# Optimization experiments

Hardware: AMD Instinct MI355X
Metric: run time of the kernel (lower is better)

Reference implementation:

```python
import jax, jax.numpy as jnp
import numpy as np

IN_CHANNELS = 3
WINDOW_SIZE = 11
SIGMA = 1.5
PAD = WINDOW_SIZE // 2


def _create_window():
    # NOTE: faithful to the original repo, the exponent is POSITIVE (a known
    # bug in AntixK/PyTorch-VAE); we replicate the exact math.
    x = np.arange(WINDOW_SIZE, dtype=np.float64)
    k = np.exp((x - WINDOW_SIZE // 2) ** 2 / (2.0 * SIGMA ** 2))
    k = (k / k.sum()).astype(np.float32)
    w2d = np.outer(k, k)  # [K, K]
    # depthwise kernel, OIHW with groups=C -> [C, 1, K, K]
    return jnp.asarray(np.broadcast_to(w2d, (IN_CHANNELS, 1, WINDOW_SIZE, WINDOW_SIZE)).copy())


def _dwconv(x, w):
    return jax.lax.conv_general_dilated(
        x, w, window_strides=(1, 1), padding=[(PAD, PAD), (PAD, PAD)],
        feature_group_count=IN_CHANNELS,
        dimension_numbers=('NCHW', 'OIHW', 'NCHW'))


def _avg_pool2(x):
    B, C, H, W = x.shape
    return x.reshape(B, C, H // 2, 2, W // 2, 2).mean(axis=(3, 5))


def _ssim(img1, img2, window):
    mu1 = _dwconv(img1, window)
    mu2 = _dwconv(img2, window)
    mu1_sq = mu1 * mu1
    mu2_sq = mu2 * mu2
    mu1_mu2 = mu1 * mu2
    sigma1_sq = _dwconv(img1 * img1, window) - mu1_sq
    sigma2_sq = _dwconv(img2 * img2, window) - mu2_sq
    sigma12 = _dwconv(img1 * img2, window) - mu1_mu2
    C1 = 0.01 ** 2
    C2 = 0.03 ** 2
    v1 = 2.0 * sigma12 + C2
    v2 = sigma1_sq + sigma2_sq + C2
    cs = jnp.mean(v1 / v2)
    ssim_map = (2.0 * mu1_mu2 + C1) * v1 / ((mu1_sq + mu2_sq + C1) * v2)
    return jnp.mean(ssim_map), cs  # size_average=True


def setup_inputs() -> dict:
    key = jax.random.key(0)
    k1, k2 = jax.random.split(key)
    shape = (32, 3, 512, 512)
    img1 = jax.random.uniform(k1, shape, dtype=jnp.float32)
    img2 = jax.random.uniform(k2, shape, dtype=jnp.float32)
    return {"img1": img1, "img2": img2}


def reference(img1, img2):
    weights = jnp.asarray([0.0448, 0.2856, 0.3001, 0.2363, 0.1333], dtype=jnp.float32)
    window = _create_window()
    mssim, mcs = [], []
    for _ in range(5):
        sim, cs = _ssim(img1, img2, window)
        mssim.append(sim)
        mcs.append(cs)
        img1 = _avg_pool2(img1)
        img2 = _avg_pool2(img2)
    mssim = jnp.stack(mssim)
    mcs = jnp.stack(mcs)
    pow1 = mcs ** weights
    pow2 = mssim ** weights
    output = jnp.prod(pow1[:-1] * pow2[-1])
    return 1.0 - output
```

## Files before the change

kernel.cpp:

```cpp
#include <hip/hip_runtime.h>
#include <cmath>

typedef short bf16x8 __attribute__((ext_vector_type(8)));
typedef float f32x4 __attribute__((ext_vector_type(4)));

struct Coeffs { float k[11]; };

__device__ __forceinline__ ushort f2bf(float f) {
    unsigned u = __float_as_uint(f);
    u += 0x7fff + ((u >> 16) & 1);
    return (ushort)(u >> 16);
}

__device__ __forceinline__ unsigned pk2(float lo, float hi) {
    unsigned d;
    asm("v_cvt_pk_bf16_f32 %0, %1, %2" : "=v"(d) : "v"(lo), "v"(hi));
    return d;
}

__device__ __forceinline__ float frcp(float x) { return __builtin_amdgcn_rcpf(x); }

__device__ __forceinline__ float4 ld4s(const float* __restrict__ p, int r, int c, int H, int W) {
    float4 v = make_float4(0.f, 0.f, 0.f, 0.f);
    if (r >= 0 && r < H) {
        const float* row = p + (size_t)r * W;
        if (c >= 0 && c + 3 < W) {
            v = *reinterpret_cast<const float4*>(row + c);
        } else {
            if (c + 0 >= 0 && c + 0 < W) v.x = row[c + 0];
            if (c + 1 >= 0 && c + 1 < W) v.y = row[c + 1];
            if (c + 2 >= 0 && c + 2 < W) v.z = row[c + 2];
            if (c + 3 >= 0 && c + 3 < W) v.w = row[c + 3];
        }
    }
    return v;
}

union FragU { ushort us[8]; bf16x8 v; uint4 q; };
union RdU   { uint4 q; bf16x8 v; };

__global__ __launch_bounds__(64)
void init_frag_kernel(uint4* __restrict__ tab, Coeffs cf) {
    const int lane = threadIdx.x;
    const int lj   = lane & 15;
    const int part = lane >> 4;
    FragU bHf, aVf;
    #pragma unroll
    for (int i = 0; i < 8; ++i) {
        const int kk = part * 8 + i;
        const int tH = kk - lj - 3;
        const int tV = kk - lj;
        float vH = 0.f, vV = 0.f;
        #pragma unroll
        for (int tt = 0; tt < 11; ++tt) {
            vH = (tH == tt) ? cf.k[tt] : vH;
            vV = (tV == tt) ? cf.k[tt] : vV;
        }
        bHf.us[i] = f2bf(vH);
        aVf.us[i] = f2bf(vV);
    }
    tab[lane]      = bHf.q;
    tab[64 + lane] = aVf.q;
}

__global__ __launch_bounds__(256)
void ssim_level0_mfma(const float* __restrict__ i1, const float* __restrict__ i2,
                      float* __restrict__ o1, float* __restrict__ o2,
                      int H, int W,
                      double* __restrict__ accum,
                      const uint4* __restrict__ frag_tab)
{
    __shared__ __align__(16) ushort A_lds[2][48][64];
    __shared__ __align__(16) ushort H_T [5][32][64];
    __shared__ double red[2][4];

    const int tid  = threadIdx.x;
    const int lane = tid & 63;
    const int lj   = lane & 15;
    const int part = lane >> 4;
    const int swz  = (lane & 7) << 4;
    const int wv   = __builtin_amdgcn_readfirstlane(tid) >> 6;

    const int bc = blockIdx.z;
    const int r0 = blockIdx.y * 32;
    const int c0 = blockIdx.x * 32;
    const float* p1 = i1 + (size_t)bc * H * W;
    const float* p2 = i2 + (size_t)bc * H * W;

    RdU bHu, aVu;
    bHu.q = frag_tab[lane];
    aVu.q = frag_tab[64 + lane];
    const bf16x8 bH = bHu.v;
    const bf16x8 aV = aVu.v;

    if (tid < 192) {
        const int row_rel = tid >> 2;
        const int colg    = tid & 3;
        const int gr  = r0 - 5 + row_rel;
        const int gc0 = c0 - 8 + 12 * colg;

        float a[12], b[12];
        if (gr >= 0 && gr < H && gc0 >= 0 && gc0 + 12 <= W) {
            const size_t idx = (size_t)gr * W + gc0;
            const float* pa = p1 + idx;
            const float* pb = p2 + idx;
            #pragma unroll
            for (int g = 0; g < 3; ++g) {
                float4 va = *reinterpret_cast<const float4*>(pa + 4 * g);
                float4 vb = *reinterpret_cast<const float4*>(pb + 4 * g);
                a[4*g+0]=va.x; a[4*g+1]=va.y; a[4*g+2]=va.z; a[4*g+3]=va.w;
                b[4*g+0]=vb.x; b[4*g+1]=vb.y; b[4*g+2]=vb.z; b[4*g+3]=vb.w;
            }
        } else {
            #pragma unroll
            for (int g = 0; g < 3; ++g) {
                float4 va = ld4s(p1, gr, gc0 + 4 * g, H, W);
                float4 vb = ld4s(p2, gr, gc0 + 4 * g, H, W);
                a[4*g+0]=va.x; a[4*g+1]=va.y; a[4*g+2]=va.z; a[4*g+3]=va.w;
                b[4*g+0]=vb.x; b[4*g+1]=vb.y; b[4*g+2]=vb.z; b[4*g+3]=vb.w;
            }
        }

        unsigned pks[2][6];
        #pragma unroll
        for (int e = 0; e < 6; ++e) {
            pks[0][e] = pk2(a[2*e], a[2*e+1]);
            pks[1][e] = pk2(b[2*e], b[2*e+1]);
        }
        const int cb   = 24 * colg;
        const int swzr = (row_rel & 7) << 4;
        char* base0 = (char*)&A_lds[0][0][0] + row_rel * 128;
        char* q0 = base0 + ((cb)      ^ swzr);
        char* q1 = base0 + ((cb + 8)  ^ swzr);
        char* q2 = base0 + ((cb + 16) ^ swzr);
        #pragma unroll
        for (int s = 0; s < 2; ++s) {
            *(uint2*)(q0 + s * 6144) = make_uint2(pks[s][0], pks[s][1]);
            *(uint2*)(q1 + s * 6144) = make_uint2(pks[s][2], pks[s][3]);
            *(uint2*)(q2 + s * 6144) = make_uint2(pks[s][4], pks[s][5]);
        }
    } else if (o1 != nullptr) {
        const int p = tid - 192;
        const int i = p & 15;
        const int h = p >> 4;
        const size_t idx = (size_t)(r0 + 2 * i) * W + (c0 + 8 * h);
        const float* pa = p1 + idx;
        const float* pb = p2 + idx;
        float4 a00 = *reinterpret_cast<const float4*>(pa);
        float4 a01 = *reinterpret_cast<const float4*>(pa + 4);
        float4 a10 = *reinterpret_cast<const float4*>(pa + W);
        float4 a11 = *reinterpret_cast<const float4*>(pa + W + 4);
        float4 b00 = *reinterpret_cast<const float4*>(pb);
        float4 b01 = *reinterpret_cast<const float4*>(pb + 4);
        float4 b10 = *reinterpret_cast<const float4*>(pb + W);
        float4 b11 = *reinterpret_cast<const float4*>(pb + W + 4);
        float4 oa, ob;
        oa.x = 0.25f*(a00.x+a00.y+a10.x+a10.y); oa.y = 0.25f*(a00.z+a00.w+a10.z+a10.w);
        oa.z = 0.25f*(a01.x+a01.y+a11.x+a11.y); oa.w = 0.25f*(a01.z+a01.w+a11.z+a11.w);
        ob.x = 0.25f*(b00.x+b00.y+b10.x+b10.y); ob.y = 0.25f*(b00.z+b00.w+b10.z+b10.w);
        ob.z = 0.25f*(b01.x+b01.y+b11.x+b11.y); ob.w = 0.25f*(b01.z+b01.w+b11.z+b11.w);
        const int W2 = W >> 1;
        const size_t base = (size_t)bc * (size_t)(H >> 1) * W2
                          + (size_t)(r0/2 + i) * W2 + (c0/2 + 4*h);
        *reinterpret_cast<float4*>(o1 + base) = oa;
        *reinterpret_cast<float4*>(o2 + base) = ob;
    }
    __syncthreads();

    const f32x4 zf = {0.f, 0.f, 0.f, 0.f};
    if (wv < 3) {
        const char* Ab = (const char*)&A_lds[0][0][0] + wv * 2048 + lj * 128;
        const char* a0p = Ab + ((part * 16)      ^ swz);
        const char* a1p = Ab + ((32 + part * 16) ^ swz);
        char* st = (char*)&H_T[0][0][0] + lj * 128 + ((wv * 32 + part * 8) ^ swz);
        #pragma unroll
        for (int cg = 0; cg < 2; ++cg) {
            const char* ap = cg ? a1p : a0p;
            uint4 da = *(const uint4*)(ap);
            uint4 db = *(const uint4*)(ap + 6144);
            unsigned wa[4] = {da.x, da.y, da.z, da.w};
            unsigned wb[4] = {db.x, db.y, db.z, db.w};
            uint4 qaa, qbb, qab;
            unsigned* paa = &qaa.x; unsigned* pbb = &qbb.x; unsigned* pab = &qab.x;
            #pragma unroll
            for (int e = 0; e < 4; ++e) {
                const float alo = __uint_as_float(wa[e] << 16);
                const float ahi = __uint_as_float(wa[e] & 0xffff0000u);
                const float blo = __uint_as_float(wb[e] << 16);
                const float bhi = __uint_as_float(wb[e] & 0xffff0000u);
                paa[e] = pk2(alo * alo, ahi * ahi);
                pbb[e] = pk2(blo * blo, bhi * bhi);
                pab[e] = pk2(alo * blo, ahi * bhi);
            }
            RdU f0, f1, f2, f3, f4;
            f0.q = da; f1.q = db; f2.q = qaa; f3.q = qbb; f4.q = qab;
            f32x4 d0 = __builtin_amdgcn_mfma_f32_16x16x32_bf16(f0.v, bH, zf, 0, 0, 0);
            f32x4 d1 = __builtin_amdgcn_mfma_f32_16x16x32_bf16(f1.v, bH, zf, 0, 0, 0);
            f32x4 d2 = __builtin_amdgcn_mfma_f32_16x16x32_bf16(f2.v, bH, zf, 0, 0, 0);
            f32x4 d3 = __builtin_amdgcn_mfma_f32_16x16x32_bf16(f3.v, bH, zf, 0, 0, 0);
            f32x4 d4 = __builtin_amdgcn_mfma_f32_16x16x32_bf16(f4.v, bH, zf, 0, 0, 0);
            char* sc = st + cg * 2048;
            *(uint2*)(sc)          = make_uint2(pk2(d0[0], d0[1]), pk2(d0[2], d0[3]));
            *(uint2*)(sc + 4096)   = make_uint2(pk2(d1[0], d1[1]), pk2(d1[2], d1[3]));
            *(uint2*)(sc + 8192)   = make_uint2(pk2(d2[0], d2[1]), pk2(d2[2], d2[3]));
            *(uint2*)(sc + 12288)  = make_uint2(pk2(d3[0], d3[1]), pk2(d3[2], d3[3]));
            *(uint2*)(sc + 16384)  = make_uint2(pk2(d4[0], d4[1]), pk2(d4[2], d4[3]));
        }
    }
    __syncthreads();

    const int rg2 = wv >> 1;
    const int cg2 = wv & 1;
    const char* hb = (const char*)&H_T[0][0][0] + cg2 * 2048 + lj * 128
                   + ((rg2 * 32 + part * 16) ^ swz);
    f32x4 acc[5];
    #pragma unroll
    for (int s = 0; s < 5; ++s) {
        RdU br;
        br.q = *(const uint4*)(hb + s * 4096);
        acc[s] = __builtin_amdgcn_mfma_f32_16x16x32_bf16(aV, br.v, zf, 0, 0, 0);
    }

    const float C1 = 1e-4f, C2 = 9e-4f;
    float ssim_acc = 0.f, cs_acc = 0.f;
    #pragma unroll
    for (int r = 0; r < 4; ++r) {
        const float mu1 = acc[0][r], mu2 = acc[1][r];
        const float m11 = acc[2][r], m22 = acc[3][r], m12 = acc[4][r];
        const float mu1s = mu1 * mu1, mu2s = mu2 * mu2, mu12 = mu1 * mu2;
        const float v1 = 2.f * (m12 - mu12) + C2;
        const float v2 = (m11 - mu1s) + (m22 - mu2s) + C2;
        const float r2 = frcp(v2);
        const float rd = frcp(mu1s + mu2s + C1);
        cs_acc   += v1 * r2;
        ssim_acc += (2.f * mu12 + C1) * v1 * r2 * rd;
    }

    #pragma unroll
    for (int off = 32; off > 0; off >>= 1) {
        ssim_acc += __shfl_down(ssim_acc, off);
        cs_acc   += __shfl_down(cs_acc, off);
    }
    if (lane == 0) { red[0][wv] = (double)ssim_acc; red[1][wv] = (double)cs_acc; }
    __syncthreads();
    if (tid == 0) {
        double s = red[0][0] + red[0][1] + red[0][2] + red[0][3];
        double c = red[1][0] + red[1][1] + red[1][2] + red[1][3];
        int slot = (blockIdx.x + blockIdx.y * 3 + blockIdx.z * 7) & 63;
        atomicAdd(&accum[slot], s);
        atomicAdd(&accum[64 + slot], c);
    }
}

__global__ __launch_bounds__(256)
void ssim_level1_mfma(const float* __restrict__ i1, const float* __restrict__ i2,
                      float* __restrict__ o1, float* __restrict__ o2,
                      int H, int W,
                      double* __restrict__ accum,
                      const uint4* __restrict__ frag_tab)
{
    __shared__ __align__(16) ushort H_T[5][32][64];
    __shared__ double red[2][4];

    const int tid  = threadIdx.x;
    const int lane = tid & 63;
    const int lj   = lane & 15;
    const int part = lane >> 4;
    const int swz  = (lane & 7) << 4;
    const int wv   = __builtin_amdgcn_readfirstlane(tid) >> 6;

    const int bc = blockIdx.z;
    const int r0 = blockIdx.y * 32;
    const int c0 = blockIdx.x * 32;
    const float* p1 = i1 + (size_t)bc * H * W;
    const float* p2 = i2 + (size_t)bc * H * W;

    RdU bHu, aVu;
    bHu.q = frag_tab[lane];
    aVu.q = frag_tab[64 + lane];
    const bf16x8 bH = bHu.v;
    const bf16x8 aV = aVu.v;

    const f32x4 zf = {0.f, 0.f, 0.f, 0.f};

    if (wv < 3) {
        const int gr = r0 - 5 + wv * 16 + lj;
        char* st = (char*)&H_T[0][0][0] + lj * 128 + ((wv * 32 + part * 8) ^ swz);
        #pragma unroll
        for (int cg = 0; cg < 2; ++cg) {
            const int gc = c0 - 8 + cg * 16 + part * 8;
            float a8[8], b8[8];
            if (gr >= 0 && gr < H && gc >= 0 && gc + 8 <= W) {
                const size_t idx = (size_t)gr * W + gc;
                float4 va0 = *reinterpret_cast<const float4*>(p1 + idx);
                float4 va1 = *reinterpret_cast<const float4*>(p1 + idx + 4);
                float4 vb0 = *reinterpret_cast<const float4*>(p2 + idx);
                float4 vb1 = *reinterpret_cast<const float4*>(p2 + idx + 4);
                a8[0]=va0.x; a8[1]=va0.y; a8[2]=va0.z; a8[3]=va0.w;
                a8[4]=va1.x; a8[5]=va1.y; a8[6]=va1.z; a8[7]=va1.w;
                b8[0]=vb0.x; b8[1]=vb0.y; b8[2]=vb0.z; b8[3]=vb0.w;
                b8[4]=vb1.x; b8[5]=vb1.y; b8[6]=vb1.z; b8[7]=vb1.w;
            } else {
                float4 va0 = ld4s(p1, gr, gc, H, W);
                float4 va1 = ld4s(p1, gr, gc + 4, H, W);
                float4 vb0 = ld4s(p2, gr, gc, H, W);
                float4 vb1 = ld4s(p2, gr, gc + 4, H, W);
                a8[0]=va0.x; a8[1]=va0.y; a8[2]=va0.z; a8[3]=va0.w;
                a8[4]=va1.x; a8[5]=va1.y; a8[6]=va1.z; a8[7]=va1.w;
                b8[0]=vb0.x; b8[1]=vb0.y; b8[2]=vb0.z; b8[3]=vb0.w;
                b8[4]=vb1.x; b8[5]=vb1.y; b8[6]=vb1.z; b8[7]=vb1.w;
            }

            unsigned pkf[5][4];
            #pragma unroll
            for (int e = 0; e < 4; ++e) {
                const float a0 = a8[2*e], a1 = a8[2*e+1];
                const float b0 = b8[2*e], b1 = b8[2*e+1];
                pkf[0][e] = pk2(a0, a1);
                pkf[1][e] = pk2(b0, b1);
                pkf[2][e] = pk2(a0*a0, a1*a1);
                pkf[3][e] = pk2(b0*b0, b1*b1);
                pkf[4][e] = pk2(a0*b0, a1*b1);
            }
            #pragma unroll
            for (int s = 0; s < 5; ++s) {
                RdU fr;
                fr.q.x = pkf[s][0]; fr.q.y = pkf[s][1];
                fr.q.z = pkf[s][2]; fr.q.w = pkf[s][3];
                f32x4 d = __builtin_amdgcn_mfma_f32_16x16x32_bf16(fr.v, bH, zf, 0, 0, 0);
                *(uint2*)(st + cg * 2048 + s * 4096)
                    = make_uint2(pk2(d[0], d[1]), pk2(d[2], d[3]));
            }
        }
    } else if (o1 != nullptr) {
        const int p = tid - 192;
        const int i = p & 15;
        const int h = p >> 4;
        const size_t idx = (size_t)(r0 + 2 * i) * W + (c0 + 8 * h);
        const float* pa = p1 + idx;
        const float* pb = p2 + idx;
        float4 a00 = *reinterpret_cast<const float4*>(pa);
        float4 a01 = *reinterpret_cast<const float4*>(pa + 4);
        float4 a10 = *reinterpret_cast<const float4*>(pa + W);
        float4 a11 = *reinterpret_cast<const float4*>(pa + W + 4);
        float4 b00 = *reinterpret_cast<const float4*>(pb);
        float4 b01 = *reinterpret_cast<const float4*>(pb + 4);
        float4 b10 = *reinterpret_cast<const float4*>(pb + W);
        float4 b11 = *reinterpret_cast<const float4*>(pb + W + 4);
        float4 oa, ob;
        oa.x = 0.25f*(a00.x+a00.y+a10.x+a10.y); oa.y = 0.25f*(a00.z+a00.w+a10.z+a10.w);
        oa.z = 0.25f*(a01.x+a01.y+a11.x+a11.y); oa.w = 0.25f*(a01.z+a01.w+a11.z+a11.w);
        ob.x = 0.25f*(b00.x+b00.y+b10.x+b10.y); ob.y = 0.25f*(b00.z+b00.w+b10.z+b10.w);
        ob.z = 0.25f*(b01.x+b01.y+b11.x+b11.y); ob.w = 0.25f*(b01.z+b01.w+b11.z+b11.w);
        const int W2 = W >> 1;
        const size_t base = (size_t)bc * (size_t)(H >> 1) * W2
                          + (size_t)(r0/2 + i) * W2 + (c0/2 + 4*h);
        *reinterpret_cast<float4*>(o1 + base) = oa;
        *reinterpret_cast<float4*>(o2 + base) = ob;
    }
    __syncthreads();

    const int rg2 = wv >> 1;
    const int cg2 = wv & 1;
    const char* hb = (const char*)&H_T[0][0][0] + cg2 * 2048 + lj * 128
                   + ((rg2 * 32 + part * 16) ^ swz);
    f32x4 acc[5];
    #pragma unroll
    for (int s = 0; s < 5; ++s) {
        RdU br;
        br.q = *(const uint4*)(hb + s * 4096);
        acc[s] = __builtin_amdgcn_mfma_f32_16x16x32_bf16(aV, br.v, zf, 0, 0, 0);
    }

    const float C1 = 1e-4f, C2 = 9e-4f;
    float ssim_acc = 0.f, cs_acc = 0.f;
    #pragma unroll
    for (int r = 0; r < 4; ++r) {
        const float mu1 = acc[0][r], mu2 = acc[1][r];
        const float m11 = acc[2][r], m22 = acc[3][r], m12 = acc[4][r];
        const float mu1s = mu1 * mu1, mu2s = mu2 * mu2, mu12 = mu1 * mu2;
        const float v1 = 2.f * (m12 - mu12) + C2;
        const float v2 = (m11 - mu1s) + (m22 - mu2s) + C2;
        const float r2 = frcp(v2);
        const float rd = frcp(mu1s + mu2s + C1);
        cs_acc   += v1 * r2;
        ssim_acc += (2.f * mu12 + C1) * v1 * r2 * rd;
    }

    #pragma unroll
    for (int off = 32; off > 0; off >>= 1) {
        ssim_acc += __shfl_down(ssim_acc, off);
        cs_acc   += __shfl_down(cs_acc, off);
    }
    if (lane == 0) { red[0][wv] = (double)ssim_acc; red[1][wv] = (double)cs_acc; }
    __syncthreads();
    if (tid == 0) {
        double s = red[0][0] + red[0][1] + red[0][2] + red[0][3];
        double c = red[1][0] + red[1][1] + red[1][2] + red[1][3];
        int slot = (blockIdx.x + blockIdx.y * 3 + blockIdx.z * 7) & 63;
        atomicAdd(&accum[slot], s);
        atomicAdd(&accum[64 + slot], c);
    }
}

#define SPF 33
#define HRF 42

__global__ __launch_bounds__(256)
void ssim_level_f32(const float* __restrict__ i1, const float* __restrict__ i2,
                    float* __restrict__ o1, float* __restrict__ o2,
                    int H, int W,
                    double* __restrict__ accum, Coeffs cf)
{
    __shared__ __align__(16) float varr[5][HRF][SPF];
    __shared__ __align__(16) float phl[2][16][16];
    __shared__ double red[2][4];

    const int tid = threadIdx.x;
    const int bc  = blockIdx.z;
    const int r0 = blockIdx.y * 32;
    const int c0 = blockIdx.x * 32;
    const float* p1 = i1 + (size_t)bc * H * W;
    const float* p2 = i2 + (size_t)bc * H * W;

    const int row_rel = tid >> 2;
    const int j  = tid & 3;
    const int cl = 8 * j;
    float hpA[4], hpB[4];
    bool pool_thread = false;

    if (tid < HRF * 4) {
        const int gr  = r0 + row_rel - 5;
        const int gcb = c0 + cl - 8;

        float a[24], b[24];
        if (gr >= 0 && gr < H && gcb >= 0 && gcb + 24 <= W) {
            const size_t idx = (size_t)gr * W + gcb;
            const float* pa = p1 + idx;
            const float* pb = p2 + idx;
            #pragma unroll
            for (int g = 0; g < 6; ++g) {
                float4 va = *reinterpret_cast<const float4*>(pa + 4 * g);
                float4 vb = *reinterpret_cast<const float4*>(pb + 4 * g);
                a[4*g+0]=va.x; a[4*g+1]=va.y; a[4*g+2]=va.z; a[4*g+3]=va.w;
                b[4*g+0]=vb.x; b[4*g+1]=vb.y; b[4*g+2]=vb.z; b[4*g+3]=vb.w;
            }
        } else {
            #pragma unroll
            for (int g = 0; g < 6; ++g) {
                float4 va = ld4s(p1, gr, gcb + 4 * g, H, W);
                float4 vb = ld4s(p2, gr, gcb + 4 * g, H, W);
                a[4*g+0]=va.x; a[4*g+1]=va.y; a[4*g+2]=va.z; a[4*g+3]=va.w;
                b[4*g+0]=vb.x; b[4*g+1]=vb.y; b[4*g+2]=vb.z; b[4*g+3]=vb.w;
            }
        }

        float acc[5][8] = {};
        #pragma unroll
        for (int i = 0; i < 24; ++i) {
            float av = a[i], bv = b[i];
            float pa2 = av * av, pb2 = bv * bv, pab = av * bv;
            #pragma unroll
            for (int jo = 0; jo < 8; ++jo) {
                const int t = i - 3 - jo;
                if (t >= 0 && t <= 10) {
                    const float kk = cf.k[t];
                    acc[0][jo] += kk * av;  acc[1][jo] += kk * bv;
                    acc[2][jo] += kk * pa2; acc[3][jo] += kk * pb2;
                    acc[4][jo] += kk * pab;
                }
            }
        }
        #pragma unroll
        for (int s = 0; s < 5; ++s) {
            *reinterpret_cast<float4*>(&varr[s][row_rel][cl]) =
                make_float4(acc[s][0], acc[s][1], acc[s][2], acc[s][3]);
            *reinterpret_cast<float4*>(&varr[s][row_rel][cl + 4]) =
                make_float4(acc[s][4], acc[s][5], acc[s][6], acc[s][7]);
        }

        if (o1 != nullptr && row_rel >= 5 && row_rel <= 36) {
            #pragma unroll
            for (int p = 0; p < 4; ++p) {
                hpA[p] = a[8 + 2*p] + a[9 + 2*p];
                hpB[p] = b[8 + 2*p] + b[9 + 2*p];
            }
            if (row_rel & 1) {
                const int i = (row_rel - 5) >> 1;
                *reinterpret_cast<float4*>(&phl[0][i][4*j]) = make_float4(hpA[0],hpA[1],hpA[2],hpA[3]);
                *reinterpret_cast<float4*>(&phl[1][i][4*j]) = make_float4(hpB[0],hpB[1],hpB[2],hpB[3]);
            } else if (row_rel >= 6) {
                pool_thread = true;
            }
        }
    }
    __syncthreads();

    if (pool_thread) {
        const int i = (row_rel - 6) >> 1;
        const int W2 = W >> 1;
        float4 qa = *reinterpret_cast<const float4*>(&phl[0][i][4*j]);
        float4 qb = *reinterpret_cast<const float4*>(&phl[1][i][4*j]);
        qa.x = 0.25f*(qa.x + hpA[0]); qa.y = 0.25f*(qa.y + hpA[1]);
        qa.z = 0.25f*(qa.z + hpA[2]); qa.w = 0.25f*(qa.w + hpA[3]);
        qb.x = 0.25f*(qb.x + hpB[0]); qb.y = 0.25f*(qb.y + hpB[1]);
        qb.z = 0.25f*(qb.z + hpB[2]); qb.w = 0.25f*(qb.w + hpB[3]);
        const size_t base = (size_t)bc * (size_t)(H >> 1) * W2
                          + (size_t)(r0/2 + i) * W2 + (c0/2 + 4*j);
        *reinterpret_cast<float4*>(o1 + base) = qa;
        *reinterpret_cast<float4*>(o2 + base) = qb;
    }

    const int col = tid & 31;
    const int rg  = tid >> 5;

    float acc[5][4] = {};
    #pragma unroll
    for (int t = 0; t < 14; ++t) {
        const int m = rg * 4 + t;
        #pragma unroll
        for (int s = 0; s < 5; ++s) {
            const float val = varr[s][m][col];
            #pragma unroll
            for (int i = 0; i < 4; ++i) {
                const int tap = t - i;
                if (tap >= 0 && tap <= 10) acc[s][i] += cf.k[tap] * val;
            }
        }
    }

    const float C1 = 1e-4f, C2 = 9e-4f;
    float ssim_acc = 0.f, cs_acc = 0.f;
    #pragma unroll
    for (int i = 0; i < 4; ++i) {
        const float mu1 = acc[0][i], mu2 = acc[1][i];
        const float m11 = acc[2][i], m22 = acc[3][i], m12 = acc[4][i];
        const float mu1s = mu1 * mu1, mu2s = mu2 * mu2, mu12 = mu1 * mu2;
        const float v1 = 2.f * (m12 - mu12) + C2;
        const float v2 = (m11 - mu1s) + (m22 - mu2s) + C2;
        const float r2 = frcp(v2);
        const float rd = frcp(mu1s + mu2s + C1);
        cs_acc   += v1 * r2;
        ssim_acc += (2.f * mu12 + C1) * v1 * r2 * rd;
    }

    #pragma unroll
    for (int off = 32; off > 0; off >>= 1) {
        ssim_acc += __shfl_down(ssim_acc, off);
        cs_acc   += __shfl_down(cs_acc, off);
    }
    const int wave = tid >> 6, lane = tid & 63;
    if (lane == 0) { red[0][wave] = (double)ssim_acc; red[1][wave] = (double)cs_acc; }
    __syncthreads();
    if (tid == 0) {
        double s = red[0][0] + red[0][1] + red[0][2] + red[0][3];
        double c = red[1][0] + red[1][1] + red[1][2] + red[1][3];
        int slot = (blockIdx.x + blockIdx.y * 3 + blockIdx.z * 7) & 63;
        atomicAdd(&accum[slot], s);
        atomicAdd(&accum[64 + slot], c);
    }
}

__global__ __launch_bounds__(64)
void finalize_kernel(const double* __restrict__ accum,
                     float* __restrict__ out, int BC)
{
    __shared__ double sums[5][2];
    int tid = threadIdx.x;
    for (int lvl = 0; lvl < 5; ++lvl) {
        for (int m = 0; m < 2; ++m) {
            double v = accum[(lvl * 2 + m) * 64 + tid];
            for (int off = 32; off > 0; off >>= 1) v += __shfl_down(v, off);
            if (tid == 0) sums[lvl][m] = v;
        }
    }
    __syncthreads();
    if (tid == 0) {
        const double w[5] = {0.0448, 0.2856, 0.3001, 0.2363, 0.1333};
        double prod = 1.0;
        for (int lvl = 0; lvl < 5; ++lvl) {
            int hw = (512 >> lvl);
            double cnt = (double)BC * (double)hw * (double)hw;
            double mssim = sums[lvl][0] / cnt;
            double mcs   = sums[lvl][1] / cnt;
            if (lvl < 4) {
                prod *= pow(mcs, w[lvl]);
            } else {
                double p2 = pow(mssim, w[4]);
                prod *= p2 * p2 * p2 * p2;
            }
        }
        out[0] = (float)(1.0 - prod);
    }
}

extern "C" void kernel_launch(void* const* d_in, const int* in_sizes, int n_in,
                              void* d_out, int out_size, void* d_ws, size_t ws_size,
                              hipStream_t stream) {
    const float* img1 = (const float*)d_in[0];
    const float* img2 = (const float*)d_in[1];
    float* out = (float*)d_out;
    char* ws = (char*)d_ws;

    const int BC = in_sizes[0] / (512 * 512);

    double* accum = (double*)ws;
    uint4*  ftab  = (uint4*)(ws + 6144);
    size_t off = 8192;
    float* lvl1[5] = {nullptr, nullptr, nullptr, nullptr, nullptr};
    float* lvl2[5] = {nullptr, nullptr, nullptr, nullptr, nullptr};
    for (int l = 1; l < 5; ++l) {
        size_t hw = (size_t)(512 >> l) * (512 >> l);
        lvl1[l] = (float*)(ws + off); off += (size_t)BC * hw * sizeof(float);
        lvl2[l] = (float*)(ws + off); off += (size_t)BC * hw * sizeof(float);
    }

    hipMemsetAsync(accum, 0, 5 * 2 * 64 * sizeof(double), stream);

    Coeffs cf;
    {
        double kd[11], sum = 0.0;
        for (int i = 0; i < 11; ++i) { kd[i] = exp(((double)((i-5)*(i-5))) / 4.5); sum += kd[i]; }
        for (int i = 0; i < 11; ++i) cf.k[i] = (float)(kd[i] / sum);
    }

    init_frag_kernel<<<1, 64, 0, stream>>>(ftab, cf);

    const float* cur1 = img1;
    const float* cur2 = img2;
    for (int lvl = 0; lvl < 5; ++lvl) {
        int H = 512 >> lvl, W = H;
        dim3 grid(W / 32, H / 32, BC);
        float* n1 = (lvl < 4) ? lvl1[lvl + 1] : nullptr;
        float* n2 = (lvl < 4) ? lvl2[lvl + 1] : nullptr;
        if (lvl == 0) {
            ssim_level0_mfma<<<grid, 256, 0, stream>>>(cur1, cur2, n1, n2, H, W,
                                                       accum + lvl * 128, ftab);
        } else if (lvl == 1) {
            ssim_level1_mfma<<<grid, 256, 0, stream>>>(cur1, cur2, n1, n2, H, W,
                                                       accum + lvl * 128, ftab);
        } else {
            ssim_level_f32<<<grid, 256, 0, stream>>>(cur1, cur2, n1, n2, H, W,
                                                     accum + lvl * 128, cf);
        }
        cur1 = n1; cur2 = n2;
    }

    finalize_kernel<<<1, 64, 0, stream>>>(accum, out, BC);
}
```

Baseline: 181.3 us.

## Process two 32-column tiles per level-0 block with software-pipelined staging

The level-0 SSIM kernel now handles a 32x64 region per block, two 32x32 tiles in sequence, and launches half as many blocks along x. The second tile's global loads are issued up front and held in registers. They are written to LDS while the vertical MFMA pass of the first tile runs, which overlaps load latency with compute. This amortizes per-block setup (fragment table loads, reduction, atomics) over more work, but raises register pressure, adds extra barriers, and halves the block count, which can reduce occupancy.

After: 160.4 us. -11.6%, faster.

```diff
diff --git a/kernel.cpp b/kernel.cpp
--- a/kernel.cpp
+++ b/kernel.cpp
@@ -63,6 +63,136 @@
     tab[64 + lane] = aVf.q;
 }
 
+__device__ __forceinline__ void stage_load(const float* __restrict__ p1,
+                                           const float* __restrict__ p2,
+                                           int H, int W, int gr, int gc0,
+                                           float (&a)[12], float (&b)[12]) {
+    if (gr >= 0 && gr < H && gc0 >= 0 && gc0 + 12 <= W) {
+        const size_t idx = (size_t)gr * W + gc0;
+        #pragma unroll
+        for (int g = 0; g < 3; ++g) {
+            float4 va = *reinterpret_cast<const float4*>(p1 + idx + 4 * g);
+            float4 vb = *reinterpret_cast<const float4*>(p2 + idx + 4 * g);
+            a[4*g+0]=va.x; a[4*g+1]=va.y; a[4*g+2]=va.z; a[4*g+3]=va.w;
+            b[4*g+0]=vb.x; b[4*g+1]=vb.y; b[4*g+2]=vb.z; b[4*g+3]=vb.w;
+        }
+    } else {
+        #pragma unroll
+        for (int g = 0; g < 3; ++g) {
+            float4 va = ld4s(p1, gr, gc0 + 4 * g, H, W);
+            float4 vb = ld4s(p2, gr, gc0 + 4 * g, H, W);
+            a[4*g+0]=va.x; a[4*g+1]=va.y; a[4*g+2]=va.z; a[4*g+3]=va.w;
+            b[4*g+0]=vb.x; b[4*g+1]=vb.y; b[4*g+2]=vb.z; b[4*g+3]=vb.w;
+        }
+    }
+}
+
+__device__ __forceinline__ void stage_write(const float (&a)[12], const float (&b)[12],
+                                            char* q0, char* q1, char* q2) {
+    unsigned pks[2][6];
+    #pragma unroll
+    for (int e = 0; e < 6; ++e) {
+        pks[0][e] = pk2(a[2*e], a[2*e+1]);
+        pks[1][e] = pk2(b[2*e], b[2*e+1]);
+    }
+    #pragma unroll
+    for (int s = 0; s < 2; ++s) {
+        *(uint2*)(q0 + s * 6144) = make_uint2(pks[s][0], pks[s][1]);
+        *(uint2*)(q1 + s * 6144) = make_uint2(pks[s][2], pks[s][3]);
+        *(uint2*)(q2 + s * 6144) = make_uint2(pks[s][4], pks[s][5]);
+    }
+}
+
+__device__ __forceinline__ void h_phase(const char* a0p, const char* a1p, char* st,
+                                        const bf16x8 bH, const f32x4 zf) {
+    #pragma unroll
+    for (int cg = 0; cg < 2; ++cg) {
+        const char* ap = cg ? a1p : a0p;
+        uint4 da = *(const uint4*)(ap);
+        uint4 db = *(const uint4*)(ap + 6144);
+        unsigned wa[4] = {da.x, da.y, da.z, da.w};
+        unsigned wb[4] = {db.x, db.y, db.z, db.w};
+        uint4 qaa, qbb, qab;
+        unsigned* paa = &qaa.x; unsigned* pbb = &qbb.x; unsigned* pab = &qab.x;
+        #pragma unroll
+        for (int e = 0; e < 4; ++e) {
+            const float alo = __uint_as_float(wa[e] << 16);
+            const float ahi = __uint_as_float(wa[e] & 0xffff0000u);
+            const float blo = __uint_as_float(wb[e] << 16);
+            const float bhi = __uint_as_float(wb[e] & 0xffff0000u);
+            paa[e] = pk2(alo * alo, ahi * ahi);
+            pbb[e] = pk2(blo * blo, bhi * bhi);
+            pab[e] = pk2(alo * blo, ahi * bhi);
+        }
+        RdU f0, f1, f2, f3, f4;
+        f0.q = da; f1.q = db; f2.q = qaa; f3.q = qbb; f4.q = qab;
+        f32x4 d0 = __builtin_amdgcn_mfma_f32_16x16x32_bf16(f0.v, bH, zf, 0, 0, 0);
+        f32x4 d1 = __builtin_amdgcn_mfma_f32_16x16x32_bf16(f1.v, bH, zf, 0, 0, 0);
+        f32x4 d2 = __builtin_amdgcn_mfma_f32_16x16x32_bf16(f2.v, bH, zf, 0, 0, 0);
+        f32x4 d3 = __builtin_amdgcn_mfma_f32_16x16x32_bf16(f3.v, bH, zf, 0, 0, 0);
+        f32x4 d4 = __builtin_amdgcn_mfma_f32_16x16x32_bf16(f4.v, bH, zf, 0, 0, 0);
+        char* sc = st + cg * 2048;
+        *(uint2*)(sc)          = make_uint2(pk2(d0[0], d0[1]), pk2(d0[2], d0[3]));
+        *(uint2*)(sc + 4096)   = make_uint2(pk2(d1[0], d1[1]), pk2(d1[2], d1[3]));
+        *(uint2*)(sc + 8192)   = make_uint2(pk2(d2[0], d2[1]), pk2(d2[2], d2[3]));
+        *(uint2*)(sc + 12288)  = make_uint2(pk2(d3[0], d3[1]), pk2(d3[2], d3[3]));
+        *(uint2*)(sc + 16384)  = make_uint2(pk2(d4[0], d4[1]), pk2(d4[2], d4[3]));
+    }
+}
+
+__device__ __forceinline__ void v_phase(const char* hb, const bf16x8 aV, const f32x4 zf,
+                                        float& ssim_acc, float& cs_acc) {
+    f32x4 acc[5];
+    #pragma unroll
+    for (int s = 0; s < 5; ++s) {
+        RdU br;
+        br.q = *(const uint4*)(hb + s * 4096);
+        acc[s] = __builtin_amdgcn_mfma_f32_16x16x32_bf16(aV, br.v, zf, 0, 0, 0);
+    }
+    const float C1 = 1e-4f, C2 = 9e-4f;
+    #pragma unroll
+    for (int r = 0; r < 4; ++r) {
+        const float mu1 = acc[0][r], mu2 = acc[1][r];
+        const float m11 = acc[2][r], m22 = acc[3][r], m12 = acc[4][r];
+        const float mu1s = mu1 * mu1, mu2s = mu2 * mu2, mu12 = mu1 * mu2;
+        const float v1 = 2.f * (m12 - mu12) + C2;
+        const float v2 = (m11 - mu1s) + (m22 - mu2s) + C2;
+        const float r2 = frcp(v2);
+        const float rd = frcp(mu1s + mu2s + C1);
+        cs_acc   += v1 * r2;
+        ssim_acc += (2.f * mu12 + C1) * v1 * r2 * rd;
+    }
+}
+
+__device__ __forceinline__ void pool_load8(const float* __restrict__ p1,
+                                           const float* __restrict__ p2,
+                                           size_t idx, int W, float4 (&P)[8]) {
+    P[0] = *reinterpret_cast<const float4*>(p1 + idx);
+    P[1] = *reinterpret_cast<const float4*>(p1 + idx + 4);
+    P[2] = *reinterpret_cast<const float4*>(p1 + idx + W);
+    P[3] = *reinterpret_cast<const float4*>(p1 + idx + W + 4);
+    P[4] = *reinterpret_cast<const float4*>(p2 + idx);
+    P[5] = *reinterpret_cast<const float4*>(p2 + idx + 4);
+    P[6] = *reinterpret_cast<const float4*>(p2 + idx + W);
+    P[7] = *reinterpret_cast<const float4*>(p2 + idx + W + 4);
+}
+
+__device__ __forceinline__ void pool_store8(const float4 (&P)[8],
+                                            float* __restrict__ o1, float* __restrict__ o2,
+                                            int bc, int H, int W, int r0, int c0t,
+                                            int i, int h) {
+    float4 oa, ob;
+    oa.x = 0.25f*(P[0].x+P[0].y+P[2].x+P[2].y); oa.y = 0.25f*(P[0].z+P[0].w+P[2].z+P[2].w);
+    oa.z = 0.25f*(P[1].x+P[1].y+P[3].x+P[3].y); oa.w = 0.25f*(P[1].z+P[1].w+P[3].z+P[3].w);
+    ob.x = 0.25f*(P[4].x+P[4].y+P[6].x+P[6].y); ob.y = 0.25f*(P[4].z+P[4].w+P[6].z+P[6].w);
+    ob.z = 0.25f*(P[5].x+P[5].y+P[7].x+P[7].y); ob.w = 0.25f*(P[5].z+P[5].w+P[7].z+P[7].w);
+    const int W2 = W >> 1;
+    const size_t base = (size_t)bc * (size_t)(H >> 1) * W2
+                      + (size_t)(r0/2 + i) * W2 + (c0t/2 + 4*h);
+    *reinterpret_cast<float4*>(o1 + base) = oa;
+    *reinterpret_cast<float4*>(o2 + base) = ob;
+}
+
 __global__ __launch_bounds__(256)
 void ssim_level0_mfma(const float* __restrict__ i1, const float* __restrict__ i2,
                       float* __restrict__ o1, float* __restrict__ o2,
@@ -83,7 +213,7 @@
 
     const int bc = blockIdx.z;
     const int r0 = blockIdx.y * 32;
-    const int c0 = blockIdx.x * 32;
+    const int c0 = blockIdx.x * 64;
     const float* p1 = i1 + (size_t)bc * H * W;
     const float* p2 = i2 + (size_t)bc * H * W;
 
@@ -92,52 +222,155 @@
     aVu.q = frag_tab[64 + lane];
     const bf16x8 bH = bHu.v;
     const bf16x8 aV = aVu.v;
-
+    const f32x4 zf = {0.f, 0.f, 0.f, 0.f};
+
+    float ssim_acc = 0.f, cs_acc = 0.f;
+
+    float aB[12], bB[12];
+    char *q0 = nullptr, *q1 = nullptr, *q2 = nullptr;
     if (tid < 192) {
         const int row_rel = tid >> 2;
         const int colg    = tid & 3;
         const int gr  = r0 - 5 + row_rel;
-        const int gc0 = c0 - 8 + 12 * colg;
-
-        float a[12], b[12];
-        if (gr >= 0 && gr < H && gc0 >= 0 && gc0 + 12 <= W) {
-            const size_t idx = (size_t)gr * W + gc0;
-            const float* pa = p1 + idx;
-            const float* pb = p2 + idx;
-            #pragma unroll
-            for (int g = 0; g < 3; ++g) {
-                float4 va = *reinterpret_cast<const float4*>(pa + 4 * g);
-                float4 vb = *reinterpret_cast<const float4*>(pb + 4 * g);
-                a[4*g+0]=va.x; a[4*g+1]=va.y; a[4*g+2]=va.z; a[4*g+3]=va.w;
-                b[4*g+0]=vb.x; b[4*g+1]=vb.y; b[4*g+2]=vb.z; b[4*g+3]=vb.w;
-            }
-        } else {
-            #pragma unroll
-            for (int g = 0; g < 3; ++g) {
-                float4 va = ld4s(p1, gr, gc0 + 4 * g, H, W);
-                float4 vb = ld4s(p2, gr, gc0 + 4 * g, H, W);
-                a[4*g+0]=va.x; a[4*g+1]=va.y; a[4*g+2]=va.z; a[4*g+3]=va.w;
-                b[4*g+0]=vb.x; b[4*g+1]=vb.y; b[4*g+2]=vb.z; b[4*g+3]=vb.w;
-            }
-        }
-
-        unsigned pks[2][6];
-        #pragma unroll
-        for (int e = 0; e < 6; ++e) {
-            pks[0][e] = pk2(a[2*e], a[2*e+1]);
-            pks[1][e] = pk2(b[2*e], b[2*e+1]);
-        }
+        const int gcA = c0 - 8 + 12 * colg;
+        float aA[12], bA[12];
+        stage_load(p1, p2, H, W, gr, gcA,      aA, bA);
+        stage_load(p1, p2, H, W, gr, gcA + 32, aB, bB);
         const int cb   = 24 * colg;
         const int swzr = (row_rel & 7) << 4;
         char* base0 = (char*)&A_lds[0][0][0] + row_rel * 128;
-        char* q0 = base0 + ((cb)      ^ swzr);
-        char* q1 = base0 + ((cb + 8)  ^ swzr);
-        char* q2 = base0 + ((cb + 16) ^ swzr);
-        #pragma unroll
-        for (int s = 0; s < 2; ++s) {
-            *(uint2*)(q0 + s * 6144) = make_uint2(pks[s][0], pks[s][1]);
-            *(uint2*)(q1 + s * 6144) = make_uint2(pks[s][2], pks[s][3]);
-            *(uint2*)(q2 + s * 6144) = make_uint2(pks[s][4], pks[s][5]);
+        q0 = base0 + ((cb)      ^ swzr);
+        q1 = base0 + ((cb + 8)  ^ swzr);
+        q2 = base0 + ((cb + 16) ^ swzr);
+        stage_write(aA, bA, q0, q1, q2);
+    } else if (o1 != nullptr) {
+        const int p = tid - 192;
+        const int i = p & 15;
+        const int h = p >> 4;
+        const size_t idxA = (size_t)(r0 + 2 * i) * W + (c0 + 8 * h);
+        float4 PA[8], PB[8];
+        pool_load8(p1, p2, idxA,      W, PA);
+        pool_load8(p1, p2, idxA + 32, W, PB);
+        pool_store8(PA, o1, o2, bc, H, W, r0, c0,      i, h);
+        pool_store8(PB, o1, o2, bc, H, W, r0, c0 + 32, i, h);
+    }
+    __syncthreads();
+
+    const char* Ab  = (const char*)&A_lds[0][0][0] + wv * 2048 + lj * 128;
+    const char* a0p = Ab + ((part * 16)      ^ swz);
+    const char* a1p = Ab + ((32 + part * 16) ^ swz);
+    char* st = (char*)&H_T[0][0][0] + lj * 128 + ((wv * 32 + part * 8) ^ swz);
+    const int rg2 = wv >> 1, cg2 = wv & 1;
+    const char* hb = (const char*)&H_T[0][0][0] + cg2 * 2048 + lj * 128
+                   + ((rg2 * 32 + part * 16) ^ swz);
+
+    if (wv < 3) h_phase(a0p, a1p, st, bH, zf);
+    __syncthreads();
+
+    if (tid < 192) stage_write(aB, bB, q0, q1, q2);
+    v_phase(hb, aV, zf, ssim_acc, cs_acc);
+    __syncthreads();
+
+    if (wv < 3) h_phase(a0p, a1p, st, bH, zf);
+    __syncthreads();
+
+    v_phase(hb, aV, zf, ssim_acc, cs_acc);
+
+    #pragma unroll
+    for (int off = 32; off > 0; off >>= 1) {
+        ssim_acc += __shfl_down(ssim_acc, off);
+        cs_acc   += __shfl_down(cs_acc, off);
+    }
+    if (lane == 0) { red[0][wv] = (double)ssim_acc; red[1][wv] = (double)cs_acc; }
+    __syncthreads();
+    if (tid == 0) {
+        double s = red[0][0] + red[0][1] + red[0][2] + red[0][3];
+        double c = red[1][0] + red[1][1] + red[1][2] + red[1][3];
+        int slot = (blockIdx.x + blockIdx.y * 3 + blockIdx.z * 7) & 63;
+        atomicAdd(&accum[slot], s);
+        atomicAdd(&accum[64 + slot], c);
+    }
+}
+
+__global__ __launch_bounds__(256)
+void ssim_level1_mfma(const float* __restrict__ i1, const float* __restrict__ i2,
+                      float* __restrict__ o1, float* __restrict__ o2,
+                      int H, int W,
+                      double* __restrict__ accum,
+                      const uint4* __restrict__ frag_tab)
+{
+    __shared__ __align__(16) ushort H_T[5][32][64];
+    __shared__ double red[2][4];
+
+    const int tid  = threadIdx.x;
+    const int lane = tid & 63;
+    const int lj   = lane & 15;
+    const int part = lane >> 4;
+    const int swz  = (lane & 7) << 4;
+    const int wv   = __builtin_amdgcn_readfirstlane(tid) >> 6;
+
+    const int bc = blockIdx.z;
+    const int r0 = blockIdx.y * 32;
+    const int c0 = blockIdx.x * 32;
+    const float* p1 = i1 + (size_t)bc * H * W;
+    const float* p2 = i2 + (size_t)bc * H * W;
+
+    RdU bHu, aVu;
+    bHu.q = frag_tab[lane];
+    aVu.q = frag_tab[64 + lane];
+    const bf16x8 bH = bHu.v;
+    const bf16x8 aV = aVu.v;
+
+    const f32x4 zf = {0.f, 0.f, 0.f, 0.f};
+
+    if (wv < 3) {
+        const int gr = r0 - 5 + wv * 16 + lj;
+        char* st = (char*)&H_T[0][0][0] + lj * 128 + ((wv * 32 + part * 8) ^ swz);
+        #pragma unroll
+        for (int cg = 0; cg < 2; ++cg) {
+            const int gc = c0 - 8 + cg * 16 + part * 8;
+            float a8[8], b8[8];
+            if (gr >= 0 && gr < H && gc >= 0 && gc + 8 <= W) {
+                const size_t idx = (size_t)gr * W + gc;
+                float4 va0 = *reinterpret_cast<const float4*>(p1 + idx);
+                float4 va1 = *reinterpret_cast<const float4*>(p1 + idx + 4);
+                float4 vb0 = *reinterpret_cast<const float4*>(p2 + idx);
+                float4 vb1 = *reinterpret_cast<const float4*>(p2 + idx + 4);
+                a8[0]=va0.x; a8[1]=va0.y; a8[2]=va0.z; a8[3]=va0.w;
+                a8[4]=va1.x; a8[5]=va1.y; a8[6]=va1.z; a8[7]=va1.w;
+                b8[0]=vb0.x; b8[1]=vb0.y; b8[2]=vb0.z; b8[3]=vb0.w;
+                b8[4]=vb1.x; b8[5]=vb1.y; b8[6]=vb1.z; b8[7]=vb1.w;
+            } else {
+                float4 va0 = ld4s(p1, gr, gc, H, W);
+                float4 va1 = ld4s(p1, gr, gc + 4, H, W);
+                float4 vb0 = ld4s(p2, gr, gc, H, W);
+                float4 vb1 = ld4s(p2, gr, gc + 4, H, W);
+                a8[0]=va0.x; a8[1]=va0.y; a8[2]=va0.z; a8[3]=va0.w;
+                a8[4]=va1.x; a8[5]=va1.y; a8[6]=va1.z; a8[7]=va1.w;
+                b8[0]=vb0.x; b8[1]=vb0.y; b8[2]=vb0.z; b8[3]=vb0.w;
+                b8[4]=vb1.x; b8[5]=vb1.y; b8[6]=vb1.z; b8[7]=vb1.w;
+            }
+
+            unsigned pkf[5][4];
+            #pragma unroll
+            for (int e = 0; e < 4; ++e) {
+                const float a0 = a8[2*e], a1 = a8[2*e+1];
+                const float b0 = b8[2*e], b1 = b8[2*e+1];
+                pkf[0][e] = pk2(a0, a1);
+                pkf[1][e] = pk2(b0, b1);
+                pkf[2][e] = pk2(a0*a0, a1*a1);
+                pkf[3][e] = pk2(b0*b0, b1*b1);
+                pkf[4][e] = pk2(a0*b0, a1*b1);
+            }
+            #pragma unroll
+            for (int s = 0; s < 5; ++s) {
+                RdU fr;
+                fr.q.x = pkf[s][0]; fr.q.y = pkf[s][1];
+                fr.q.z = pkf[s][2]; fr.q.w = pkf[s][3];
+                f32x4 d = __builtin_amdgcn_mfma_f32_16x16x32_bf16(fr.v, bH, zf, 0, 0, 0);
+                *(uint2*)(st + cg * 2048 + s * 4096)
+                    = make_uint2(pk2(d[0], d[1]), pk2(d[2], d[3]));
+            }
         }
     } else if (o1 != nullptr) {
         const int p = tid - 192;
@@ -167,199 +400,6 @@
     }
     __syncthreads();
 
-    const f32x4 zf = {0.f, 0.f, 0.f, 0.f};
-    if (wv < 3) {
-        const char* Ab = (const char*)&A_lds[0][0][0] + wv * 2048 + lj * 128;
-        const char* a0p = Ab + ((part * 16)      ^ swz);
-        const char* a1p = Ab + ((32 + part * 16) ^ swz);
-        char* st = (char*)&H_T[0][0][0] + lj * 128 + ((wv * 32 + part * 8) ^ swz);
-        #pragma unroll
-        for (int cg = 0; cg < 2; ++cg) {
-            const char* ap = cg ? a1p : a0p;
-            uint4 da = *(const uint4*)(ap);
-            uint4 db = *(const uint4*)(ap + 6144);
-            unsigned wa[4] = {da.x, da.y, da.z, da.w};
-            unsigned wb[4] = {db.x, db.y, db.z, db.w};
-            uint4 qaa, qbb, qab;
-            unsigned* paa = &qaa.x; unsigned* pbb = &qbb.x; unsigned* pab = &qab.x;
-            #pragma unroll
-            for (int e = 0; e < 4; ++e) {
-                const float alo = __uint_as_float(wa[e] << 16);
-                const float ahi = __uint_as_float(wa[e] & 0xffff0000u);
-                const float blo = __uint_as_float(wb[e] << 16);
-                const float bhi = __uint_as_float(wb[e] & 0xffff0000u);
-                paa[e] = pk2(alo * alo, ahi * ahi);
-                pbb[e] = pk2(blo * blo, bhi * bhi);
-                pab[e] = pk2(alo * blo, ahi * bhi);
-            }
-            RdU f0, f1, f2, f3, f4;
-            f0.q = da; f1.q = db; f2.q = qaa; f3.q = qbb; f4.q = qab;
-            f32x4 d0 = __builtin_amdgcn_mfma_f32_16x16x32_bf16(f0.v, bH, zf, 0, 0, 0);
-            f32x4 d1 = __builtin_amdgcn_mfma_f32_16x16x32_bf16(f1.v, bH, zf, 0, 0, 0);
-            f32x4 d2 = __builtin_amdgcn_mfma_f32_16x16x32_bf16(f2.v, bH, zf, 0, 0, 0);
-            f32x4 d3 = __builtin_amdgcn_mfma_f32_16x16x32_bf16(f3.v, bH, zf, 0, 0, 0);
-            f32x4 d4 = __builtin_amdgcn_mfma_f32_16x16x32_bf16(f4.v, bH, zf, 0, 0, 0);
-            char* sc = st + cg * 2048;
-            *(uint2*)(sc)          = make_uint2(pk2(d0[0], d0[1]), pk2(d0[2], d0[3]));
-            *(uint2*)(sc + 4096)   = make_uint2(pk2(d1[0], d1[1]), pk2(d1[2], d1[3]));
-            *(uint2*)(sc + 8192)   = make_uint2(pk2(d2[0], d2[1]), pk2(d2[2], d2[3]));
-            *(uint2*)(sc + 12288)  = make_uint2(pk2(d3[0], d3[1]), pk2(d3[2], d3[3]));
-            *(uint2*)(sc + 16384)  = make_uint2(pk2(d4[0], d4[1]), pk2(d4[2], d4[3]));
-        }
-    }
-    __syncthreads();
-
-    const int rg2 = wv >> 1;
-    const int cg2 = wv & 1;
-    const char* hb = (const char*)&H_T[0][0][0] + cg2 * 2048 + lj * 128
-                   + ((rg2 * 32 + part * 16) ^ swz);
-    f32x4 acc[5];
-    #pragma unroll
-    for (int s = 0; s < 5; ++s) {
-        RdU br;
-        br.q = *(const uint4*)(hb + s * 4096);
-        acc[s] = __builtin_amdgcn_mfma_f32_16x16x32_bf16(aV, br.v, zf, 0, 0, 0);
-    }
-
-    const float C1 = 1e-4f, C2 = 9e-4f;
-    float ssim_acc = 0.f, cs_acc = 0.f;
-    #pragma unroll
-    for (int r = 0; r < 4; ++r) {
-        const float mu1 = acc[0][r], mu2 = acc[1][r];
-        const float m11 = acc[2][r], m22 = acc[3][r], m12 = acc[4][r];
-        const float mu1s = mu1 * mu1, mu2s = mu2 * mu2, mu12 = mu1 * mu2;
-        const float v1 = 2.f * (m12 - mu12) + C2;
-        const float v2 = (m11 - mu1s) + (m22 - mu2s) + C2;
-        const float r2 = frcp(v2);
-        const float rd = frcp(mu1s + mu2s + C1);
-        cs_acc   += v1 * r2;
-        ssim_acc += (2.f * mu12 + C1) * v1 * r2 * rd;
-    }
-
-    #pragma unroll
-    for (int off = 32; off > 0; off >>= 1) {
-        ssim_acc += __shfl_down(ssim_acc, off);
-        cs_acc   += __shfl_down(cs_acc, off);
-    }
-    if (lane == 0) { red[0][wv] = (double)ssim_acc; red[1][wv] = (double)cs_acc; }
-    __syncthreads();
-    if (tid == 0) {
-        double s = red[0][0] + red[0][1] + red[0][2] + red[0][3];
-        double c = red[1][0] + red[1][1] + red[1][2] + red[1][3];
-        int slot = (blockIdx.x + blockIdx.y * 3 + blockIdx.z * 7) & 63;
-        atomicAdd(&accum[slot], s);
-        atomicAdd(&accum[64 + slot], c);
-    }
-}
-
-__global__ __launch_bounds__(256)
-void ssim_level1_mfma(const float* __restrict__ i1, const float* __restrict__ i2,
-                      float* __restrict__ o1, float* __restrict__ o2,
-                      int H, int W,
-                      double* __restrict__ accum,
-                      const uint4* __restrict__ frag_tab)
-{
-    __shared__ __align__(16) ushort H_T[5][32][64];
-    __shared__ double red[2][4];
-
-    const int tid  = threadIdx.x;
-    const int lane = tid & 63;
-    const int lj   = lane & 15;
-    const int part = lane >> 4;
-    const int swz  = (lane & 7) << 4;
-    const int wv   = __builtin_amdgcn_readfirstlane(tid) >> 6;
-
-    const int bc = blockIdx.z;
-    const int r0 = blockIdx.y * 32;
-    const int c0 = blockIdx.x * 32;
-    const float* p1 = i1 + (size_t)bc * H * W;
-    const float* p2 = i2 + (size_t)bc * H * W;
-
-    RdU bHu, aVu;
-    bHu.q = frag_tab[lane];
-    aVu.q = frag_tab[64 + lane];
-    const bf16x8 bH = bHu.v;
-    const bf16x8 aV = aVu.v;
-
-    const f32x4 zf = {0.f, 0.f, 0.f, 0.f};
-
-    if (wv < 3) {
-        const int gr = r0 - 5 + wv * 16 + lj;
-        char* st = (char*)&H_T[0][0][0] + lj * 128 + ((wv * 32 + part * 8) ^ swz);
-        #pragma unroll
-        for (int cg = 0; cg < 2; ++cg) {
-            const int gc = c0 - 8 + cg * 16 + part * 8;
-            float a8[8], b8[8];
-            if (gr >= 0 && gr < H && gc >= 0 && gc + 8 <= W) {
-                const size_t idx = (size_t)gr * W + gc;
-                float4 va0 = *reinterpret_cast<const float4*>(p1 + idx);
-                float4 va1 = *reinterpret_cast<const float4*>(p1 + idx + 4);
-                float4 vb0 = *reinterpret_cast<const float4*>(p2 + idx);
-                float4 vb1 = *reinterpret_cast<const float4*>(p2 + idx + 4);
-                a8[0]=va0.x; a8[1]=va0.y; a8[2]=va0.z; a8[3]=va0.w;
-                a8[4]=va1.x; a8[5]=va1.y; a8[6]=va1.z; a8[7]=va1.w;
-                b8[0]=vb0.x; b8[1]=vb0.y; b8[2]=vb0.z; b8[3]=vb0.w;
-                b8[4]=vb1.x; b8[5]=vb1.y; b8[6]=vb1.z; b8[7]=vb1.w;
-            } else {
-                float4 va0 = ld4s(p1, gr, gc, H, W);
-                float4 va1 = ld4s(p1, gr, gc + 4, H, W);
-                float4 vb0 = ld4s(p2, gr, gc, H, W);
-                float4 vb1 = ld4s(p2, gr, gc + 4, H, W);
-                a8[0]=va0.x; a8[1]=va0.y; a8[2]=va0.z; a8[3]=va0.w;
-                a8[4]=va1.x; a8[5]=va1.y; a8[6]=va1.z; a8[7]=va1.w;
-                b8[0]=vb0.x; b8[1]=vb0.y; b8[2]=vb0.z; b8[3]=vb0.w;
-                b8[4]=vb1.x; b8[5]=vb1.y; b8[6]=vb1.z; b8[7]=vb1.w;
-            }
-
-            unsigned pkf[5][4];
-            #pragma unroll
-            for (int e = 0; e < 4; ++e) {
-                const float a0 = a8[2*e], a1 = a8[2*e+1];
-                const float b0 = b8[2*e], b1 = b8[2*e+1];
-                pkf[0][e] = pk2(a0, a1);
-                pkf[1][e] = pk2(b0, b1);
-                pkf[2][e] = pk2(a0*a0, a1*a1);
-                pkf[3][e] = pk2(b0*b0, b1*b1);
-                pkf[4][e] = pk2(a0*b0, a1*b1);
-            }
-            #pragma unroll
-            for (int s = 0; s < 5; ++s) {
-                RdU fr;
-                fr.q.x = pkf[s][0]; fr.q.y = pkf[s][1];
-                fr.q.z = pkf[s][2]; fr.q.w = pkf[s][3];
-                f32x4 d = __builtin_amdgcn_mfma_f32_16x16x32_bf16(fr.v, bH, zf, 0, 0, 0);
-                *(uint2*)(st + cg * 2048 + s * 4096)
-                    = make_uint2(pk2(d[0], d[1]), pk2(d[2], d[3]));
-            }
-        }
-    } else if (o1 != nullptr) {
-        const int p = tid - 192;
-        const int i = p & 15;
-        const int h = p >> 4;
-        const size_t idx = (size_t)(r0 + 2 * i) * W + (c0 + 8 * h);
-        const float* pa = p1 + idx;
-        const float* pb = p2 + idx;
-        float4 a00 = *reinterpret_cast<const float4*>(pa);
-        float4 a01 = *reinterpret_cast<const float4*>(pa + 4);
-        float4 a10 = *reinterpret_cast<const float4*>(pa + W);
-        float4 a11 = *reinterpret_cast<const float4*>(pa + W + 4);
-        float4 b00 = *reinterpret_cast<const float4*>(pb);
-        float4 b01 = *reinterpret_cast<const float4*>(pb + 4);
-        float4 b10 = *reinterpret_cast<const float4*>(pb + W);
-        float4 b11 = *reinterpret_cast<const float4*>(pb + W + 4);
-        float4 oa, ob;
-        oa.x = 0.25f*(a00.x+a00.y+a10.x+a10.y); oa.y = 0.25f*(a00.z+a00.w+a10.z+a10.w);
-        oa.z = 0.25f*(a01.x+a01.y+a11.x+a11.y); oa.w = 0.25f*(a01.z+a01.w+a11.z+a11.w);
-        ob.x = 0.25f*(b00.x+b00.y+b10.x+b10.y); ob.y = 0.25f*(b00.z+b00.w+b10.z+b10.w);
-        ob.z = 0.25f*(b01.x+b01.y+b11.x+b11.y); ob.w = 0.25f*(b01.z+b01.w+b11.z+b11.w);
-        const int W2 = W >> 1;
-        const size_t base = (size_t)bc * (size_t)(H >> 1) * W2
-                          + (size_t)(r0/2 + i) * W2 + (c0/2 + 4*h);
-        *reinterpret_cast<float4*>(o1 + base) = oa;
-        *reinterpret_cast<float4*>(o2 + base) = ob;
-    }
-    __syncthreads();
-
     const int rg2 = wv >> 1;
     const int cg2 = wv & 1;
     const char* hb = (const char*)&H_T[0][0][0] + cg2 * 2048 + lj * 128
@@ -630,16 +670,18 @@
     const float* cur2 = img2;
     for (int lvl = 0; lvl < 5; ++lvl) {
         int H = 512 >> lvl, W = H;
-        dim3 grid(W / 32, H / 32, BC);
         float* n1 = (lvl < 4) ? lvl1[lvl + 1] : nullptr;
         float* n2 = (lvl < 4) ? lvl2[lvl + 1] : nullptr;
         if (lvl == 0) {
+            dim3 grid(W / 64, H / 32, BC);
             ssim_level0_mfma<<<grid, 256, 0, stream>>>(cur1, cur2, n1, n2, H, W,
                                                        accum + lvl * 128, ftab);
         } else if (lvl == 1) {
+            dim3 grid(W / 32, H / 32, BC);
             ssim_level1_mfma<<<grid, 256, 0, stream>>>(cur1, cur2, n1, n2, H, W,
                                                        accum + lvl * 128, ftab);
         } else {
+            dim3 grid(W / 32, H / 32, BC);
             ssim_level_f32<<<grid, 256, 0, stream>>>(cur1, cur2, n1, n2, H, W,
                                                      accum + lvl * 128, cf);
         }
```
